# Performance work log

Hardware: AMD Instinct MI355X
Metric: run time of the kernel (lower is better)

The kernel has to match this reference:

```python
import jax, jax.numpy as jnp
import numpy as np

NUM_USERS = 100000
NUM_ITEMS = 50000
N_TOTAL = NUM_USERS + NUM_ITEMS
NNZ = 4000000
LATENT_DIM = 64
N_LAYERS = 3
BATCH = 16384


def setup_inputs() -> dict:
    key = jax.random.key(0)
    k1, k2, k3, k4, k5, k6, k7 = jax.random.split(key, 7)
    return {
        "user_emb": jax.random.normal(k1, (NUM_USERS, LATENT_DIM), dtype=jnp.float32) * 0.1,
        "item_emb": jax.random.normal(k2, (NUM_ITEMS, LATENT_DIM), dtype=jnp.float32) * 0.1,
        "vals": jax.random.uniform(k3, (NNZ,), dtype=jnp.float32),
        "rows": jax.random.randint(k4, (NNZ,), 0, N_TOTAL, dtype=jnp.int32),
        "cols": jax.random.randint(k5, (NNZ,), 0, N_TOTAL, dtype=jnp.int32),
        "users": jax.random.randint(k6, (BATCH,), 0, NUM_USERS, dtype=jnp.int64),
        "items": jax.random.randint(k7, (BATCH,), 0, NUM_ITEMS, dtype=jnp.int64),
    }


def _spmm(vals, rows, cols, x):
    # sparse.mm(A, x) with A given as COO edge list: out[r] += vals * x[c]
    return jax.ops.segment_sum(vals[:, None] * x[cols], rows, num_segments=N_TOTAL)


def reference(user_emb, item_emb, vals, rows, cols, users, items):
    # LightGCN.computer(): multi-hop propagation + mean over layer outputs
    all_emb = jnp.concatenate([user_emb, item_emb], axis=0)  # [N+M, d]
    acc = all_emb
    emb = all_emb
    for _ in range(N_LAYERS):
        emb = _spmm(vals, rows, cols, emb)
        acc = acc + emb
    light_out = acc / jnp.asarray(N_LAYERS + 1, dtype=acc.dtype)
    all_users = light_out[:NUM_USERS]
    all_items = light_out[NUM_USERS:]
    # forward(users, items): gather and elementwise dot product
    u = all_users[users]  # [B, d]
    i = all_items[items]  # [B, d]
    gamma = jnp.sum(u * i, axis=1)  # [B]
    return gamma
```

## Files before the change

kernel.cpp:

```cpp
#include <hip/hip_runtime.h>

#define NUM_USERS 100000
#define NUM_ITEMS 50000
#define N_TOTAL   150000
#define LATENT    64
#define BATCH     16384
#define BROWS     512
#define NB        293
#define CAP       16384
#define P1_T      512
#define P1_C      4096

typedef unsigned int u32;
typedef unsigned short u16;

__device__ __forceinline__ u16 f32_to_bf16(float f) {
    u32 u = __float_as_uint(f);
    u32 r = (u + 0x7FFFu + ((u >> 16) & 1u)) >> 16;
    return (u16)r;
}
__device__ __forceinline__ float bf16_lo(u32 w) { return __uint_as_float(w << 16); }
__device__ __forceinline__ float bf16_hi(u32 w) { return __uint_as_float(w & 0xFFFF0000u); }

__device__ __forceinline__ void fma4(float acc[4], uint2 xv, float v) {
    acc[0] = fmaf(v, bf16_lo(xv.x), acc[0]);
    acc[1] = fmaf(v, bf16_hi(xv.x), acc[1]);
    acc[2] = fmaf(v, bf16_lo(xv.y), acc[2]);
    acc[3] = fmaf(v, bf16_hi(xv.y), acc[3]);
}

__global__ void __launch_bounds__(P1_T)
partition1_kernel(const int* __restrict__ rows, const int* __restrict__ cols,
                  const float* __restrict__ vals,
                  int* __restrict__ ccur, uint2* __restrict__ packed0, int nnz) {
    __shared__ u32 skey[P1_C];
    __shared__ u32 sval[P1_C];
    __shared__ u16 sbucket[P1_C];
    __shared__ int cnt[NB];
    __shared__ int lstart[NB];
    __shared__ int lcur[NB];
    __shared__ int gbase[NB];
    __shared__ int scanbuf[P1_T];

    int t = threadIdx.x;
    int base = blockIdx.x * P1_C;
    int chunkN = nnz - base; if (chunkN > P1_C) chunkN = P1_C;

    for (int i = t; i < NB; i += P1_T) cnt[i] = 0;
    __syncthreads();

    int er[8]; u32 ek[8]; u32 ev[8];
    #pragma unroll
    for (int k = 0; k < 8; ++k) {
        int e = base + k * P1_T + t;
        bool ok = (k * P1_T + t) < chunkN;
        int r = ok ? rows[e] : 0;
        er[k] = ok ? (r >> 9) : -1;
        if (ok) {
            ek[k] = (u32)cols[e] | ((u32)(r & (BROWS - 1)) << 18);
            ev[k] = __float_as_uint(vals[e]);
            atomicAdd(&cnt[er[k]], 1);
        }
    }
    __syncthreads();

    int v = (t < NB) ? cnt[t] : 0;
    scanbuf[t] = v;
    __syncthreads();
    for (int d = 1; d < P1_T; d <<= 1) {
        int x = (t >= d) ? scanbuf[t - d] : 0;
        __syncthreads();
        scanbuf[t] += x;
        __syncthreads();
    }
    if (t < NB) {
        int excl = scanbuf[t] - v;
        lstart[t] = excl;
        lcur[t] = excl;
        gbase[t] = v ? atomicAdd(&ccur[t], v) : 0;
    }
    __syncthreads();

    #pragma unroll
    for (int k = 0; k < 8; ++k) {
        if (er[k] >= 0) {
            int pos = atomicAdd(&lcur[er[k]], 1);
            skey[pos] = ek[k];
            sval[pos] = ev[k];
            sbucket[pos] = (u16)er[k];
        }
    }
    __syncthreads();

    for (int idx = t; idx < chunkN; idx += P1_T) {
        int b2 = sbucket[idx];
        size_t gp = (size_t)b2 * CAP + gbase[b2] + (idx - lstart[b2]);
        packed0[gp] = make_uint2(skey[idx], sval[idx]);
    }
}

__global__ void bucket_scan_kernel(const int* __restrict__ ccur, int* __restrict__ cptr,
                                   int* __restrict__ rowptr, int nnz) {
    __shared__ int s[512];
    int t = threadIdx.x;
    int v = (t < NB) ? ccur[t] : 0;
    s[t] = v;
    __syncthreads();
    for (int d = 1; d < 512; d <<= 1) {
        int x = (t >= d) ? s[t - d] : 0;
        __syncthreads();
        s[t] += x;
        __syncthreads();
    }
    if (t < NB) cptr[t] = s[t] - v;
    if (t == 0) { cptr[NB] = nnz; rowptr[N_TOTAL] = nnz; }
}

__global__ void __launch_bounds__(BROWS)
partition2_kernel(const int* __restrict__ cptr, const uint2* __restrict__ packed0,
                  uint2* __restrict__ edges, int* __restrict__ rowptr) {
    __shared__ int cnt[BROWS];
    __shared__ int s[BROWS];
    __shared__ int cur[BROWS];
    int b = blockIdx.x;
    int t = threadIdx.x;
    const uint2* src = packed0 + (size_t)b * CAP;
    int outb = cptr[b];
    int count = cptr[b + 1] - outb;
    cnt[t] = 0;
    __syncthreads();
    for (int i = t; i < count; i += 2 * BROWS) {
        u32 k0 = src[i].x >> 18;
        int i2 = i + BROWS;
        if (i2 < count) {
            u32 k1 = src[i2].x >> 18;
            atomicAdd(&cnt[k0], 1);
            atomicAdd(&cnt[k1], 1);
        } else {
            atomicAdd(&cnt[k0], 1);
        }
    }
    __syncthreads();
    int v = cnt[t];
    s[t] = v;
    __syncthreads();
    for (int d = 1; d < BROWS; d <<= 1) {
        int x = (t >= d) ? s[t - d] : 0;
        __syncthreads();
        s[t] += x;
        __syncthreads();
    }
    int excl = s[t] - v;
    cur[t] = excl;
    int r = (b << 9) + t;
    if (r < N_TOTAL) rowptr[r] = outb + excl;
    __syncthreads();
    for (int i = t; i < count; i += 2 * BROWS) {
        uint2 p0 = src[i];
        int i2 = i + BROWS;
        if (i2 < count) {
            uint2 p1 = src[i2];
            int pos0 = outb + atomicAdd(&cur[p0.x >> 18], 1);
            int pos1 = outb + atomicAdd(&cur[p1.x >> 18], 1);
            edges[pos0] = make_uint2(p0.x & 0x3FFFFu, p0.y);
            edges[pos1] = make_uint2(p1.x & 0x3FFFFu, p1.y);
        } else {
            int pos0 = outb + atomicAdd(&cur[p0.x >> 18], 1);
            edges[pos0] = make_uint2(p0.x & 0x3FFFFu, p0.y);
        }
    }
}

__global__ void convert_kernel(const float* __restrict__ ue, const float* __restrict__ ie,
                               u16* __restrict__ x) {
    int i = blockIdx.x * blockDim.x + threadIdx.x;
    if (i >= N_TOTAL * LATENT) return;
    float f = (i < NUM_USERS * LATENT) ? ue[i] : ie[i - NUM_USERS * LATENT];
    x[i] = f32_to_bf16(f);
}

__device__ __forceinline__ void row_tail(const uint2* __restrict__ edges,
                                         const u16* __restrict__ x,
                                         int i, int e, int j, int q, float acc[4]) {
    for (; i + 8 <= e; i += 8) {
        uint2 e0 = edges[i + j];
        uint2 e1 = edges[i + 4 + j];
        uint2 x0 = *reinterpret_cast<const uint2*>(x + (size_t)e0.x * LATENT + q);
        uint2 x1 = *reinterpret_cast<const uint2*>(x + (size_t)e1.x * LATENT + q);
        fma4(acc, x0, __uint_as_float(e0.y));
        fma4(acc, x1, __uint_as_float(e1.y));
    }
    for (; i < e; i += 4) {
        uint2 e0 = edges[i + j];
        float v0 = (i + j < e) ? __uint_as_float(e0.y) : 0.f;
        uint2 x0 = *reinterpret_cast<const uint2*>(x + (size_t)e0.x * LATENT + q);
        fma4(acc, x0, v0);
    }
}

__device__ __forceinline__ void spmm_row(const uint2* __restrict__ edges,
                                         const u16* __restrict__ x,
                                         int s, int e, int lane, float acc[4]) {
    int j = lane >> 4;
    int q = (lane & 15) << 2;
    acc[0] = acc[1] = acc[2] = acc[3] = 0.f;
    int i = s;
    for (; i + 16 <= e; i += 16) {
        uint2 e0 = edges[i + j];
        uint2 e1 = edges[i + 4 + j];
        uint2 e2 = edges[i + 8 + j];
        uint2 e3 = edges[i + 12 + j];
        uint2 x0 = *reinterpret_cast<const uint2*>(x + (size_t)e0.x * LATENT + q);
        uint2 x1 = *reinterpret_cast<const uint2*>(x + (size_t)e1.x * LATENT + q);
        uint2 x2 = *reinterpret_cast<const uint2*>(x + (size_t)e2.x * LATENT + q);
        uint2 x3 = *reinterpret_cast<const uint2*>(x + (size_t)e3.x * LATENT + q);
        fma4(acc, x0, __uint_as_float(e0.y));
        fma4(acc, x1, __uint_as_float(e1.y));
        fma4(acc, x2, __uint_as_float(e2.y));
        fma4(acc, x3, __uint_as_float(e3.y));
    }
    row_tail(edges, x, i, e, j, q, acc);
    #pragma unroll
    for (int k = 0; k < 4; ++k) {
        acc[k] += __shfl_xor(acc[k], 16, 64);
        acc[k] += __shfl_xor(acc[k], 32, 64);
    }
}

__global__ void spmm_kernel(const int* __restrict__ rowptr, const uint2* __restrict__ edges,
                            const u16* __restrict__ x, u16* __restrict__ y) {
    int wid = blockIdx.x * 4 + (threadIdx.x >> 6);
    int r0 = wid * 2;
    int lane = threadIdx.x & 63;
    int j = lane >> 4;
    int q = (lane & 15) << 2;
    int i0 = rowptr[r0];
    int e0 = rowptr[r0 + 1];
    int i1 = e0;
    int e1 = rowptr[r0 + 2];
    float a0[4] = {0.f, 0.f, 0.f, 0.f};
    float a1[4] = {0.f, 0.f, 0.f, 0.f};

    while (i0 + 8 <= e0 && i1 + 8 <= e1) {
        uint2 p00 = edges[i0 + j];
        uint2 p01 = edges[i0 + 4 + j];
        uint2 p10 = edges[i1 + j];
        uint2 p11 = edges[i1 + 4 + j];
        uint2 g00 = *reinterpret_cast<const uint2*>(x + (size_t)p00.x * LATENT + q);
        uint2 g01 = *reinterpret_cast<const uint2*>(x + (size_t)p01.x * LATENT + q);
        uint2 g10 = *reinterpret_cast<const uint2*>(x + (size_t)p10.x * LATENT + q);
        uint2 g11 = *reinterpret_cast<const uint2*>(x + (size_t)p11.x * LATENT + q);
        fma4(a0, g00, __uint_as_float(p00.y));
        fma4(a0, g01, __uint_as_float(p01.y));
        fma4(a1, g10, __uint_as_float(p10.y));
        fma4(a1, g11, __uint_as_float(p11.y));
        i0 += 8;
        i1 += 8;
    }
    row_tail(edges, x, i0, e0, j, q, a0);
    row_tail(edges, x, i1, e1, j, q, a1);

    #pragma unroll
    for (int k = 0; k < 4; ++k) {
        a0[k] += __shfl_xor(a0[k], 16, 64);
        a0[k] += __shfl_xor(a0[k], 32, 64);
        a1[k] += __shfl_xor(a1[k], 16, 64);
        a1[k] += __shfl_xor(a1[k], 32, 64);
    }
    if (lane < 16) {
        u32 w0 = (u32)f32_to_bf16(a0[0]) | ((u32)f32_to_bf16(a0[1]) << 16);
        u32 w1 = (u32)f32_to_bf16(a0[2]) | ((u32)f32_to_bf16(a0[3]) << 16);
        *reinterpret_cast<uint2*>(y + (size_t)r0 * LATENT + (lane << 2)) = make_uint2(w0, w1);
        u32 w2 = (u32)f32_to_bf16(a1[0]) | ((u32)f32_to_bf16(a1[1]) << 16);
        u32 w3 = (u32)f32_to_bf16(a1[2]) | ((u32)f32_to_bf16(a1[3]) << 16);
        *reinterpret_cast<uint2*>(y + (size_t)(r0 + 1) * LATENT + (lane << 2)) = make_uint2(w2, w3);
    }
}

__global__ void spmm_batch_kernel(const int* __restrict__ rowptr, const uint2* __restrict__ edges,
                                  const u16* __restrict__ x,
                                  const int* __restrict__ users, const int* __restrict__ items,
                                  float* __restrict__ u_acc, float* __restrict__ i_acc) {
    int slot = blockIdx.x * 4 + (threadIdx.x >> 6);
    int lane = threadIdx.x & 63;
    int row = (slot < BATCH) ? users[slot] : (NUM_USERS + items[slot - BATCH]);
    int s = rowptr[row], e = rowptr[row + 1];
    float acc[4];
    spmm_row(edges, x, s, e, lane, acc);
    if (lane < 16) {
        float* dst = (slot < BATCH) ? (u_acc + (size_t)slot * LATENT)
                                    : (i_acc + (size_t)(slot - BATCH) * LATENT);
        float4* p = reinterpret_cast<float4*>(dst + (lane << 2));
        float4 old = *p;
        *p = make_float4(old.x + acc[0], old.y + acc[1], old.z + acc[2], old.w + acc[3]);
    }
}

__global__ void init_acc_kernel(const float* __restrict__ user_emb,
                                const float* __restrict__ item_emb,
                                const int* __restrict__ users,
                                const int* __restrict__ items,
                                float* __restrict__ u_acc,
                                float* __restrict__ i_acc) {
    int tid = blockIdx.x * blockDim.x + threadIdx.x;
    int b = tid >> 6, d = tid & 63;
    if (b >= BATCH) return;
    u_acc[tid] = user_emb[(size_t)users[b] * LATENT + d];
    i_acc[tid] = item_emb[(size_t)items[b] * LATENT + d];
}

__global__ void gather_acc_kernel(const u16* __restrict__ emb,
                                  const int* __restrict__ users,
                                  const int* __restrict__ items,
                                  float* __restrict__ u_acc,
                                  float* __restrict__ i_acc) {
    int tid = blockIdx.x * blockDim.x + threadIdx.x;
    int b = tid >> 6, d = tid & 63;
    if (b >= BATCH) return;
    u_acc[tid] += __uint_as_float(((u32)emb[(size_t)users[b] * LATENT + d]) << 16);
    i_acc[tid] += __uint_as_float(((u32)emb[((size_t)items[b] + NUM_USERS) * LATENT + d]) << 16);
}

__global__ void dot_kernel(const float* __restrict__ u_acc,
                           const float* __restrict__ i_acc,
                           float* __restrict__ out) {
    int b = blockIdx.x;
    int d = threadIdx.x;
    float p = u_acc[b * 64 + d] * i_acc[b * 64 + d];
    #pragma unroll
    for (int off = 32; off; off >>= 1) p += __shfl_down(p, off, 64);
    if (d == 0) out[b] = p * (1.0f / 16.0f);
}

extern "C" void kernel_launch(void* const* d_in, const int* in_sizes, int n_in,
                              void* d_out, int out_size, void* d_ws, size_t ws_size,
                              hipStream_t stream) {
    const float* user_emb = (const float*)d_in[0];
    const float* item_emb = (const float*)d_in[1];
    const float* vals     = (const float*)d_in[2];
    const int*   rows     = (const int*)d_in[3];
    const int*   cols     = (const int*)d_in[4];
    const int*   users    = (const int*)d_in[5];
    const int*   items    = (const int*)d_in[6];
    float* out = (float*)d_out;

    const int nnz = in_sizes[2];

    char* ws = (char*)d_ws;
    const size_t embB   = (size_t)N_TOTAL * LATENT * sizeof(u16);
    const size_t accB   = (size_t)BATCH * LATENT * sizeof(float);
    const size_t slabB  = (size_t)NB * CAP * sizeof(uint2);
    const size_t edgeB  = (size_t)(nnz + 16) * sizeof(uint2);

    size_t off = 0;
    u16*   emb_a   = (u16*)  (ws + off); off += embB;
    u16*   emb_b   = (u16*)  (ws + off); off += embB;
    uint2* packed0 = (uint2*)(ws + off); off += slabB;
    uint2* edges   = (uint2*)(ws + off); off += edgeB;
    float* u_acc   = (float*)(ws + off); off += accB;
    float* i_acc   = (float*)(ws + off); off += accB;
    int*   rowptr  = (int*)  (ws + off); off += (size_t)(N_TOTAL + 1) * sizeof(int);
    int*   ccur    = (int*)  (ws + off); off += (size_t)(NB + 1) * sizeof(int);
    int*   cptr    = (int*)  (ws + off); off += (size_t)(NB + 1) * sizeof(int);

    hipMemsetAsync(ccur, 0, (size_t)(NB + 1) * sizeof(int), stream);
    hipMemsetAsync(edges + nnz, 0, 16 * sizeof(uint2), stream);
    partition1_kernel<<<(nnz + P1_C - 1) / P1_C, P1_T, 0, stream>>>(
        rows, cols, vals, ccur, packed0, nnz);
    bucket_scan_kernel<<<1, 512, 0, stream>>>(ccur, cptr, rowptr, nnz);
    partition2_kernel<<<NB, BROWS, 0, stream>>>(cptr, packed0, edges, rowptr);

    convert_kernel<<<(N_TOTAL * LATENT + 255) / 256, 256, 0, stream>>>(user_emb, item_emb, emb_a);
    init_acc_kernel<<<(BATCH * 64) / 256, 256, 0, stream>>>(
        user_emb, item_emb, users, items, u_acc, i_acc);

    u16* cur = emb_a;
    u16* nxt = emb_b;
    for (int l = 0; l < 2; ++l) {
        spmm_kernel<<<N_TOTAL / 8, 256, 0, stream>>>(rowptr, edges, cur, nxt);
        gather_acc_kernel<<<(BATCH * 64) / 256, 256, 0, stream>>>(
            nxt, users, items, u_acc, i_acc);
        u16* t = cur; cur = nxt; nxt = t;
    }

    spmm_batch_kernel<<<(2 * BATCH) / 4, 256, 0, stream>>>(
        rowptr, edges, cur, users, items, u_acc, i_acc);

    dot_kernel<<<BATCH, 64, 0, stream>>>(u_acc, i_acc, out);
}
```

Baseline: 311.9 us.

## Use wave-shuffle scans, separate row-label array, and vectorize bf16 conversion

Replaces the shared-memory Hillis-Steele block scans in the partition and bucket-scan kernels with a wave-shuffle scan plus an 8-entry cross-wave fixup, cutting the number of barriers. Partition1 also writes a compact u16 local-row label array, so partition2's counting pass reads 2 bytes per edge instead of 8. The bf16 convert kernel now handles four floats per thread using float4 loads and ushort4 stores. The cost is an extra global write per edge in partition1 and more workspace.

```diff
diff --git a/kernel.cpp b/kernel.cpp
--- a/kernel.cpp
+++ b/kernel.cpp
@@ -29,10 +29,34 @@
     acc[3] = fmaf(v, bf16_hi(xv.y), acc[3]);
 }
 
+__device__ __forceinline__ int wave_incl_scan(int v, int lane) {
+    #pragma unroll
+    for (int d = 1; d < 64; d <<= 1) {
+        int t = __shfl_up(v, d, 64);
+        if (lane >= d) v += t;
+    }
+    return v;
+}
+
+__device__ __forceinline__ int block_excl_scan_512(int v, int t, int* wsum) {
+    int lane = t & 63, w = t >> 6;
+    int incl = wave_incl_scan(v, lane);
+    if (lane == 63) wsum[w] = incl;
+    __syncthreads();
+    if (t == 0) {
+        int acc = 0;
+        #pragma unroll
+        for (int k = 0; k < 8; ++k) { int c = wsum[k]; wsum[k] = acc; acc += c; }
+    }
+    __syncthreads();
+    return wsum[w] + incl - v;
+}
+
 __global__ void __launch_bounds__(P1_T)
 partition1_kernel(const int* __restrict__ rows, const int* __restrict__ cols,
                   const float* __restrict__ vals,
-                  int* __restrict__ ccur, uint2* __restrict__ packed0, int nnz) {
+                  int* __restrict__ ccur, uint2* __restrict__ packed0,
+                  u16* __restrict__ klab, int nnz) {
     __shared__ u32 skey[P1_C];
     __shared__ u32 sval[P1_C];
     __shared__ u16 sbucket[P1_C];
@@ -40,7 +64,7 @@
     __shared__ int lstart[NB];
     __shared__ int lcur[NB];
     __shared__ int gbase[NB];
-    __shared__ int scanbuf[P1_T];
+    __shared__ int wsum[8];
 
     int t = threadIdx.x;
     int base = blockIdx.x * P1_C;
@@ -65,16 +89,8 @@
     __syncthreads();
 
     int v = (t < NB) ? cnt[t] : 0;
-    scanbuf[t] = v;
-    __syncthreads();
-    for (int d = 1; d < P1_T; d <<= 1) {
-        int x = (t >= d) ? scanbuf[t - d] : 0;
-        __syncthreads();
-        scanbuf[t] += x;
-        __syncthreads();
-    }
+    int excl = block_excl_scan_512(v, t, wsum);
     if (t < NB) {
-        int excl = scanbuf[t] - v;
         lstart[t] = excl;
         lcur[t] = excl;
         gbase[t] = v ? atomicAdd(&ccur[t], v) : 0;
@@ -95,45 +111,42 @@
     for (int idx = t; idx < chunkN; idx += P1_T) {
         int b2 = sbucket[idx];
         size_t gp = (size_t)b2 * CAP + gbase[b2] + (idx - lstart[b2]);
-        packed0[gp] = make_uint2(skey[idx], sval[idx]);
+        u32 key = skey[idx];
+        packed0[gp] = make_uint2(key, sval[idx]);
+        klab[gp] = (u16)(key >> 18);
     }
 }
 
 __global__ void bucket_scan_kernel(const int* __restrict__ ccur, int* __restrict__ cptr,
                                    int* __restrict__ rowptr, int nnz) {
-    __shared__ int s[512];
+    __shared__ int wsum[8];
     int t = threadIdx.x;
     int v = (t < NB) ? ccur[t] : 0;
-    s[t] = v;
-    __syncthreads();
-    for (int d = 1; d < 512; d <<= 1) {
-        int x = (t >= d) ? s[t - d] : 0;
-        __syncthreads();
-        s[t] += x;
-        __syncthreads();
-    }
-    if (t < NB) cptr[t] = s[t] - v;
+    int excl = block_excl_scan_512(v, t, wsum);
+    if (t < NB) cptr[t] = excl;
     if (t == 0) { cptr[NB] = nnz; rowptr[N_TOTAL] = nnz; }
 }
 
 __global__ void __launch_bounds__(BROWS)
 partition2_kernel(const int* __restrict__ cptr, const uint2* __restrict__ packed0,
+                  const u16* __restrict__ klab,
                   uint2* __restrict__ edges, int* __restrict__ rowptr) {
     __shared__ int cnt[BROWS];
-    __shared__ int s[BROWS];
     __shared__ int cur[BROWS];
+    __shared__ int wsum[8];
     int b = blockIdx.x;
     int t = threadIdx.x;
     const uint2* src = packed0 + (size_t)b * CAP;
+    const u16*   kl  = klab + (size_t)b * CAP;
     int outb = cptr[b];
     int count = cptr[b + 1] - outb;
     cnt[t] = 0;
     __syncthreads();
     for (int i = t; i < count; i += 2 * BROWS) {
-        u32 k0 = src[i].x >> 18;
+        u16 k0 = kl[i];
         int i2 = i + BROWS;
         if (i2 < count) {
-            u32 k1 = src[i2].x >> 18;
+            u16 k1 = kl[i2];
             atomicAdd(&cnt[k0], 1);
             atomicAdd(&cnt[k1], 1);
         } else {
@@ -142,15 +155,7 @@
     }
     __syncthreads();
     int v = cnt[t];
-    s[t] = v;
-    __syncthreads();
-    for (int d = 1; d < BROWS; d <<= 1) {
-        int x = (t >= d) ? s[t - d] : 0;
-        __syncthreads();
-        s[t] += x;
-        __syncthreads();
-    }
-    int excl = s[t] - v;
+    int excl = block_excl_scan_512(v, t, wsum);
     cur[t] = excl;
     int r = (b << 9) + t;
     if (r < N_TOTAL) rowptr[r] = outb + excl;
@@ -174,9 +179,15 @@
 __global__ void convert_kernel(const float* __restrict__ ue, const float* __restrict__ ie,
                                u16* __restrict__ x) {
     int i = blockIdx.x * blockDim.x + threadIdx.x;
-    if (i >= N_TOTAL * LATENT) return;
-    float f = (i < NUM_USERS * LATENT) ? ue[i] : ie[i - NUM_USERS * LATENT];
-    x[i] = f32_to_bf16(f);
+    const int n4 = N_TOTAL * LATENT / 4;
+    const int ub = NUM_USERS * LATENT / 4;
+    if (i >= n4) return;
+    float4 f = (i < ub) ? reinterpret_cast<const float4*>(ue)[i]
+                        : reinterpret_cast<const float4*>(ie)[i - ub];
+    ushort4 o;
+    o.x = f32_to_bf16(f.x); o.y = f32_to_bf16(f.y);
+    o.z = f32_to_bf16(f.z); o.w = f32_to_bf16(f.w);
+    reinterpret_cast<ushort4*>(x)[i] = o;
 }
 
 __device__ __forceinline__ void row_tail(const uint2* __restrict__ edges,
@@ -350,12 +361,14 @@
     const size_t embB   = (size_t)N_TOTAL * LATENT * sizeof(u16);
     const size_t accB   = (size_t)BATCH * LATENT * sizeof(float);
     const size_t slabB  = (size_t)NB * CAP * sizeof(uint2);
+    const size_t klabB  = (size_t)NB * CAP * sizeof(u16);
     const size_t edgeB  = (size_t)(nnz + 16) * sizeof(uint2);
 
     size_t off = 0;
     u16*   emb_a   = (u16*)  (ws + off); off += embB;
     u16*   emb_b   = (u16*)  (ws + off); off += embB;
     uint2* packed0 = (uint2*)(ws + off); off += slabB;
+    u16*   klab    = (u16*)  (ws + off); off += klabB;
     uint2* edges   = (uint2*)(ws + off); off += edgeB;
     float* u_acc   = (float*)(ws + off); off += accB;
     float* i_acc   = (float*)(ws + off); off += accB;
@@ -366,11 +379,12 @@
     hipMemsetAsync(ccur, 0, (size_t)(NB + 1) * sizeof(int), stream);
     hipMemsetAsync(edges + nnz, 0, 16 * sizeof(uint2), stream);
     partition1_kernel<<<(nnz + P1_C - 1) / P1_C, P1_T, 0, stream>>>(
-        rows, cols, vals, ccur, packed0, nnz);
+        rows, cols, vals, ccur, packed0, klab, nnz);
     bucket_scan_kernel<<<1, 512, 0, stream>>>(ccur, cptr, rowptr, nnz);
-    partition2_kernel<<<NB, BROWS, 0, stream>>>(cptr, packed0, edges, rowptr);
-
-    convert_kernel<<<(N_TOTAL * LATENT + 255) / 256, 256, 0, stream>>>(user_emb, item_emb, emb_a);
+    partition2_kernel<<<NB, BROWS, 0, stream>>>(cptr, packed0, klab, edges, rowptr);
+
+    convert_kernel<<<(N_TOTAL * LATENT / 4 + 255) / 256, 256, 0, stream>>>(
+        user_emb, item_emb, emb_a);
     init_acc_kernel<<<(BATCH * 64) / 256, 256, 0, stream>>>(
         user_emb, item_emb, users, items, u_acc, i_acc);
 
```

Result: faster. 304.7 us (-2.3%).
